# Performance work log

Hardware: AMD Instinct MI355X
Metric: run time of the kernel (lower is better)

## Reference

```python
import jax, jax.numpy as jnp
import numpy as np

HIDDEN = 768
MLP_HIDDEN = 3072
HEADS = 12
HEAD_DIM = HIDDEN // HEADS

def setup_inputs() -> dict:
    key = jax.random.key(0)
    ks = jax.random.split(key, 12)
    s = 0.02
    return {
        "x": jax.random.normal(ks[0], (16, 1024, HIDDEN), dtype=jnp.float32),
        "ln1_g": jnp.ones((HIDDEN,), jnp.float32),
        "ln1_b": jnp.zeros((HIDDEN,), jnp.float32),
        "wq": jax.random.normal(ks[1], (HIDDEN, HIDDEN), jnp.float32) * s,
        "wk": jax.random.normal(ks[2], (HIDDEN, HIDDEN), jnp.float32) * s,
        "wv": jax.random.normal(ks[3], (HIDDEN, HIDDEN), jnp.float32) * s,
        "wo": jax.random.normal(ks[4], (HIDDEN, HIDDEN), jnp.float32) * s,
        "bo": jnp.zeros((HIDDEN,), jnp.float32),
        "ln2_g": jnp.ones((HIDDEN,), jnp.float32),
        "ln2_b": jnp.zeros((HIDDEN,), jnp.float32),
        "w1": jax.random.normal(ks[5], (HIDDEN, MLP_HIDDEN), jnp.float32) * s,
        "b1": jnp.zeros((MLP_HIDDEN,), jnp.float32),
        "w2": jax.random.normal(ks[6], (MLP_HIDDEN, HIDDEN), jnp.float32) * s,
        "b2": jnp.zeros((HIDDEN,), jnp.float32),
    }

def _layernorm(x, g, b, eps=1e-5):
    mu = jnp.mean(x, axis=-1, keepdims=True)
    var = jnp.mean(jnp.square(x - mu), axis=-1, keepdims=True)
    return (x - mu) * jax.lax.rsqrt(var + eps) * g + b

def reference(x, ln1_g, ln1_b, wq, wk, wv, wo, bo, ln2_g, ln2_b, w1, b1, w2, b2):
    b, n, _ = x.shape
    h, d = HEADS, HEAD_DIM
    scale = d ** -0.5
    # Attention branch
    xn = _layernorm(x, ln1_g, ln1_b)
    q = (xn @ wq.T).reshape(b, n, h, d).transpose(0, 2, 1, 3)  # bhnd
    k = (xn @ wk.T).reshape(b, n, h, d).transpose(0, 2, 1, 3)
    v = (xn @ wv.T).reshape(b, n, h, d).transpose(0, 2, 1, 3)
    score = jax.nn.softmax(jnp.einsum('bhif,bhjf->bhij', q, k) * scale, axis=-1)
    attn = jnp.einsum('bhij,bhjf->bihf', score, v).reshape(b, n, h * d)
    x = attn @ wo.T + bo + x
    # MLP branch
    xn = _layernorm(x, ln2_g, ln2_b)
    hdn = jax.nn.gelu(xn @ w1 + b1, approximate=False)
    x = hdn @ w2 + b2 + x
    return x
```

## Files before the change

### kernel.cpp

```cpp
#include <hip/hip_runtime.h>
#include <hip/hip_bf16.h>

#define HIDDEN 768
#define MLPH   3072
#define HEADS  12
#define HD     64
#define SEQ    1024
#define BATCH  16
#define MTOT   (BATCH*SEQ)

typedef __attribute__((ext_vector_type(8))) short  short8;
typedef __attribute__((ext_vector_type(8))) __bf16 bf16x8;
typedef __attribute__((ext_vector_type(4))) float  floatx4;

#define CL2 0.18033688011112042f

__device__ inline short f2bf(float f) {
  __hip_bfloat16 h = __float2bfloat16(f);
  return *reinterpret_cast<short*>(&h);
}

__device__ inline floatx4 mfma_bf16(short8 a, short8 b, floatx4 c) {
  return __builtin_amdgcn_mfma_f32_16x16x32_bf16(
      __builtin_bit_cast(bf16x8, a), __builtin_bit_cast(bf16x8, b), c, 0, 0, 0);
}

__device__ inline void gl_lds16(const short* g, short* l) {
  __builtin_amdgcn_global_load_lds(
      (const __attribute__((address_space(1))) unsigned int*)g,
      (__attribute__((address_space(3))) unsigned int*)l, 16, 0, 0);
}

__global__ __launch_bounds__(256) void conv_weights(
    const float* __restrict__ wq, const float* __restrict__ wk,
    const float* __restrict__ wv, const float* __restrict__ wo,
    const float* __restrict__ w1, const float* __restrict__ w2,
    short* __restrict__ wqkvb, short* __restrict__ wob,
    short* __restrict__ w1t,   short* __restrict__ w2t)
{
  int i = blockIdx.x * 256 + threadIdx.x;
  const int HH = HIDDEN * HIDDEN;
  if (i < HH) {
    wqkvb[i]        = f2bf(wq[i]);
    wqkvb[HH + i]   = f2bf(wk[i]);
    wqkvb[2*HH + i] = f2bf(wv[i]);
    wob[i]          = f2bf(wo[i]);
  }
  if (i < HIDDEN * MLPH) {
    int n = i / HIDDEN, k = i % HIDDEN;
    w1t[i] = f2bf(w1[(size_t)k * MLPH + n]);
    int n2 = i / MLPH, k2 = i % MLPH;
    w2t[i] = f2bf(w2[(size_t)k2 * HIDDEN + n2]);
  }
}

__global__ __launch_bounds__(256) void ln_kernel(
    const float* __restrict__ x, const float* __restrict__ g,
    const float* __restrict__ b, short* __restrict__ out)
{
  int row = blockIdx.x;
  const float* xr = x + (size_t)row * HIDDEN;
  int t = threadIdx.x;
  float v0 = xr[t], v1 = xr[t + 256], v2 = xr[t + 512];
  float s  = v0 + v1 + v2;
  float s2 = v0*v0 + v1*v1 + v2*v2;
  for (int off = 32; off > 0; off >>= 1) {
    s  += __shfl_down(s, off);
    s2 += __shfl_down(s2, off);
  }
  __shared__ float red[8];
  __shared__ float stats[2];
  int wave = t >> 6;
  if ((t & 63) == 0) { red[wave] = s; red[4 + wave] = s2; }
  __syncthreads();
  if (t == 0) {
    float S  = red[0] + red[1] + red[2] + red[3];
    float S2 = red[4] + red[5] + red[6] + red[7];
    float mu  = S * (1.0f / HIDDEN);
    float var = S2 * (1.0f / HIDDEN) - mu * mu;
    stats[0] = mu;
    stats[1] = rsqrtf(var + 1e-5f);
  }
  __syncthreads();
  float mu = stats[0], rs = stats[1];
  short* orow = out + (size_t)row * HIDDEN;
  orow[t]       = f2bf((v0 - mu) * rs * g[t]       + b[t]);
  orow[t + 256] = f2bf((v1 - mu) * rs * g[t + 256] + b[t + 256]);
  orow[t + 512] = f2bf((v2 - mu) * rs * g[t + 512] + b[t + 512]);
}

template<int OUTMODE , bool BIAS, bool GELU_E, bool RES,
         bool SCALEQ = false>
__global__ __launch_bounds__(512, 2) void gemm_bt2(
    const short* __restrict__ A, const short* __restrict__ B,
    const float* __restrict__ bias, const float* __restrict__ res,
    void* __restrict__ out, int M, int N, int K)
{
  __shared__ alignas(16) short As[2][8192];
  __shared__ alignas(16) short Bs[2][8192];

  int tid = threadIdx.x;
  int lane = tid & 63, wave = tid >> 6;
  int wr = wave >> 2, wc = wave & 3;
  int quad = lane >> 4, lc = lane & 15;

  int nbx = gridDim.x;
  int nwg = nbx * gridDim.y;
  int orig = blockIdx.y * nbx + blockIdx.x;
  int q8 = nwg >> 3, r8 = nwg & 7;
  int xcd = orig & 7, sub = orig >> 3;
  int wg = (xcd < r8 ? xcd * (q8 + 1) : r8 * (q8 + 1) + (xcd - r8) * q8) + sub;
  int m0 = (wg / nbx) * 256;
  int n0 = (wg % nbx) * 256;

  int srow = tid >> 2;
  int skb  = (tid & 3) ^ ((srow >> 1) & 3);
  const short* ga0 = A + (size_t)(m0 + srow) * K + skb * 8;
  const short* ga1 = ga0 + (size_t)128 * K;
  const short* gb0 = B + (size_t)(n0 + srow) * K + skb * 8;
  const short* gb1 = gb0 + (size_t)128 * K;
  int lbase = wave * 512;

#define STAGE(KO, BUF) {                              \
    gl_lds16(ga0 + (KO), &As[BUF][lbase]);            \
    gl_lds16(ga1 + (KO), &As[BUF][4096 + lbase]);     \
    gl_lds16(gb0 + (KO), &Bs[BUF][lbase]);            \
    gl_lds16(gb1 + (KO), &Bs[BUF][4096 + lbase]);     \
  }

  floatx4 acc[8][4];
#pragma unroll
  for (int i = 0; i < 8; ++i)
#pragma unroll
    for (int j = 0; j < 4; ++j) acc[i][j] = floatx4{0.f, 0.f, 0.f, 0.f};

  int apos = (quad ^ ((lc >> 1) & 3)) * 8;
  int arow = wr * 128 + lc;
  int brow = wc * 64 + lc;

#define COMPUTE(BUF) {                                                  \
    const short* as_ = As[BUF];                                         \
    const short* bs_ = Bs[BUF];                                         \
    short8 af[8], bfr[4];                                               \
    _Pragma("unroll")                                                   \
    for (int i = 0; i < 8; ++i)                                         \
      af[i] = *(const short8*)&as_[(arow + i * 16) * 32 + apos];        \
    _Pragma("unroll")                                                   \
    for (int j = 0; j < 4; ++j)                                         \
      bfr[j] = *(const short8*)&bs_[(brow + j * 16) * 32 + apos];       \
    _Pragma("unroll")                                                   \
    for (int i = 0; i < 8; ++i)                                         \
      _Pragma("unroll")                                                 \
      for (int j = 0; j < 4; ++j)                                       \
        acc[i][j] = mfma_bf16(af[i], bfr[j], acc[i][j]);                \
  }

  int NT = K >> 5;

  STAGE(0, 0);
  __syncthreads();

  for (int t = 0; t < NT; t += 2) {
    STAGE((t + 1) * 32, 1);
    COMPUTE(0);
    __syncthreads();
    if (t + 2 < NT) STAGE((t + 2) * 32, 0);
    COMPUTE(1);
    __syncthreads();
  }
#undef STAGE
#undef COMPUTE

#pragma unroll
  for (int i = 0; i < 8; ++i)
#pragma unroll
    for (int j = 0; j < 4; ++j)
#pragma unroll
      for (int r = 0; r < 4; ++r) {
        int row = m0 + wr * 128 + i * 16 + quad * 4 + r;
        int col = n0 + wc * 64 + j * 16 + lc;
        float v = acc[i][j][r];
        if (BIAS)   v += bias[col];
        if (GELU_E) v = 0.5f * v * (1.0f + erff(v * 0.70710678118f));
        if (RES)    v += res[(size_t)row * N + col];
        if (SCALEQ && col < HIDDEN) v *= CL2;
        if (OUTMODE == 1) ((short*)out)[(size_t)row * N + col] = f2bf(v);
        else              ((float*)out)[(size_t)row * N + col] = v;
      }
}

__global__ __launch_bounds__(256) void attn_kernel(
    const short* __restrict__ qkv, short* __restrict__ out)
{
  int qt = blockIdx.x;
  int h  = blockIdx.y;
  int b  = blockIdx.z;
  int tid = threadIdx.x, lane = tid & 63, wave = tid >> 6;
  int quad = lane >> 4, lc = lane & 15;

  __shared__ alignas(16) short Qs[2 * 64 * 32];
  __shared__ alignas(16) short Ks[2 * 64 * 32];
  __shared__ alignas(16) unsigned int Vt[64 * 32];
  __shared__ alignas(16) short Ps[4][16 * 64];

  const int LDQ = 3 * HIDDEN;
  const short* qb = qkv + (size_t)(b * SEQ) * LDQ + h * HD;
  const short* kb = qb + HIDDEN;
  const short* vb = qb + 2 * HIDDEN;

  {
    int r_l = lane >> 2, lcb = lane & 3;
    int kblk = lcb ^ ((r_l >> 1) & 3);
#pragma unroll
    for (int t = 0; t < 2; ++t) {
      const short* g = qb + (size_t)(qt * 64 + wave * 16 + r_l) * LDQ + t * 32 + kblk * 8;
      gl_lds16(g, &Qs[t * 2048 + (wave * 16) * 32]);
    }
  }
  __syncthreads();

  short8 aq[2];
#pragma unroll
  for (int ks = 0; ks < 2; ++ks) {
    int pos = quad ^ ((lc >> 1) & 3);
    aq[ks] = *(const short8*)&Qs[ks * 2048 + (wave * 16 + lc) * 32 + pos * 8];
  }

  floatx4 oacc[4];
#pragma unroll
  for (int n2 = 0; n2 < 4; ++n2) oacc[n2] = floatx4{0.f, 0.f, 0.f, 0.f};
  float l_r[4] = {0.f, 0.f, 0.f, 0.f};

  int rt = tid >> 3;
  int ct = tid & 7;

  for (int kt = 0; kt < 16; ++kt) {
    {
      int r_l = lane >> 2, lcb = lane & 3;
      int kblk = lcb ^ ((r_l >> 1) & 3);
#pragma unroll
      for (int t = 0; t < 2; ++t) {
        const short* g = kb + (size_t)(kt * 64 + wave * 16 + r_l) * LDQ + t * 32 + kblk * 8;
        gl_lds16(g, &Ks[t * 2048 + (wave * 16) * 32]);
      }
      const short* gv = vb + (size_t)(kt * 64 + 2 * rt) * LDQ + ct * 8;
      short8 v0 = *(const short8*)(gv);
      short8 v1 = *(const short8*)(gv + LDQ);
      int posv = (rt >> 2) ^ ct;
#pragma unroll
      for (int j = 0; j < 8; ++j) {
        unsigned int d = ((unsigned int)(unsigned short)v1[j] << 16) |
                          (unsigned int)(unsigned short)v0[j];
        Vt[(ct * 8 + j) * 32 + posv * 4 + (rt & 3)] = d;
      }
    }
    __syncthreads();

    floatx4 sacc[4];
#pragma unroll
    for (int n2 = 0; n2 < 4; ++n2) sacc[n2] = floatx4{0.f, 0.f, 0.f, 0.f};
#pragma unroll
    for (int ks = 0; ks < 2; ++ks) {
#pragma unroll
      for (int n2 = 0; n2 < 4; ++n2) {
        int pos = quad ^ ((lc >> 1) & 3);
        short8 bk = *(const short8*)&Ks[ks * 2048 + (n2 * 16 + lc) * 32 + pos * 8];
        sacc[n2] = mfma_bf16(aq[ks], bk, sacc[n2]);
      }
    }

#pragma unroll
    for (int r = 0; r < 4; ++r) {
      int row = quad * 4 + r;
      float p0 = exp2f(sacc[0][r]);
      float p1 = exp2f(sacc[1][r]);
      float p2 = exp2f(sacc[2][r]);
      float p3 = exp2f(sacc[3][r]);
      l_r[r] += (p0 + p1) + (p2 + p3);
      float pv[4] = {p0, p1, p2, p3};
#pragma unroll
      for (int n2 = 0; n2 < 4; ++n2) {
        int tbw  = 2 * n2 + (lc >> 3);
        int posw = tbw ^ (row & 7);
        Ps[wave][row * 64 + posw * 8 + (lc & 7)] = f2bf(pv[n2]);
      }
    }
    __syncthreads();

#pragma unroll
    for (int ks = 0; ks < 2; ++ks) {
      int posp = (ks * 4 + quad) ^ (lc & 7);
      short8 ap = *(const short8*)&Ps[wave][lc * 64 + posp * 8];
#pragma unroll
      for (int n2 = 0; n2 < 4; ++n2) {
        int c = n2 * 16 + lc;
        int posr = ((ks * 4 + quad) ^ ((c >> 3) & 7));
        short8 bv = *(const short8*)&Vt[c * 32 + posr * 4];
        oacc[n2] = mfma_bf16(ap, bv, oacc[n2]);
      }
    }
    __syncthreads();
  }

#pragma unroll
  for (int r = 0; r < 4; ++r) {
    float rs = l_r[r];
#pragma unroll
    for (int off = 1; off < 16; off <<= 1)
      rs += __shfl_xor(rs, off);
    float inv = 1.0f / rs;
    int row = b * SEQ + qt * 64 + wave * 16 + quad * 4 + r;
#pragma unroll
    for (int n2 = 0; n2 < 4; ++n2) {
      int col = h * HD + n2 * 16 + lc;
      out[(size_t)row * HIDDEN + col] = f2bf(oacc[n2][r] * inv);
    }
  }
}

extern "C" void kernel_launch(void* const* d_in, const int* in_sizes, int n_in,
                              void* d_out, int out_size, void* d_ws, size_t ws_size,
                              hipStream_t stream) {
  const float* x    = (const float*)d_in[0];
  const float* ln1g = (const float*)d_in[1];
  const float* ln1b = (const float*)d_in[2];
  const float* wq   = (const float*)d_in[3];
  const float* wk   = (const float*)d_in[4];
  const float* wv   = (const float*)d_in[5];
  const float* wo   = (const float*)d_in[6];
  const float* bo   = (const float*)d_in[7];
  const float* ln2g = (const float*)d_in[8];
  const float* ln2b = (const float*)d_in[9];
  const float* w1   = (const float*)d_in[10];
  const float* b1   = (const float*)d_in[11];
  const float* w2   = (const float*)d_in[12];
  const float* b2   = (const float*)d_in[13];

  auto rup = [](size_t b) { return (b + 255) & ~(size_t)255; };
  const size_t wbytes = rup((size_t)3 * HIDDEN * HIDDEN * 2) +
                        rup((size_t)HIDDEN * HIDDEN * 2) +
                        rup((size_t)MLPH * HIDDEN * 2) +
                        rup((size_t)HIDDEN * MLPH * 2);

  int R = SEQ;
  const int cands[4] = {16384, 8192, 4096, 2048};
  for (int i = 0; i < 4; ++i) {
    size_t need = wbytes + rup((size_t)cands[i] * 1536) + rup((size_t)cands[i] * 6144);
    if (need <= ws_size) { R = cands[i]; break; }
  }

  char* ws = (char*)d_ws;
  size_t off = 0;
  auto alloc = [&](size_t bytes) {
    char* p = ws + off;
    off += (bytes + 255) & ~(size_t)255;
    return p;
  };
  short* wqkvb = (short*)alloc((size_t)3 * HIDDEN * HIDDEN * 2);
  short* wob   = (short*)alloc((size_t)HIDDEN * HIDDEN * 2);
  short* w1t   = (short*)alloc((size_t)MLPH * HIDDEN * 2);
  short* w2t   = (short*)alloc((size_t)HIDDEN * MLPH * 2);
  short* slotA = (short*)alloc((size_t)R * 1536);
  short* bigR  = (short*)alloc((size_t)R * 6144);

  conv_weights<<<(HIDDEN * MLPH + 255) / 256, 256, 0, stream>>>(
      wq, wk, wv, wo, w1, w2, wqkvb, wob, w1t, w2t);

  const int nch = MTOT / R;
  for (int c = 0; c < nch; ++c) {
    const float* xc  = x + (size_t)c * R * HIDDEN;
    float*       x2c = (float*)d_out + (size_t)c * R * HIDDEN;

    ln_kernel<<<R, 256, 0, stream>>>(xc, ln1g, ln1b, slotA);
    gemm_bt2<1, false, false, false, true>
        <<<dim3((3 * HIDDEN) / 256, R / 256), 512, 0, stream>>>(
        slotA, wqkvb, nullptr, nullptr, bigR, R, 3 * HIDDEN, HIDDEN);
    attn_kernel<<<dim3(SEQ / 64, HEADS, R / SEQ), 256, 0, stream>>>(bigR, slotA);
    gemm_bt2<0, true, false, true>
        <<<dim3(HIDDEN / 256, R / 256), 512, 0, stream>>>(
        slotA, wob, bo, xc, x2c, R, HIDDEN, HIDDEN);
    ln_kernel<<<R, 256, 0, stream>>>(x2c, ln2g, ln2b, slotA);
    gemm_bt2<1, true, true, false>
        <<<dim3(MLPH / 256, R / 256), 512, 0, stream>>>(
        slotA, w1t, b1, nullptr, bigR, R, MLPH, HIDDEN);
    gemm_bt2<0, true, false, true>
        <<<dim3(HIDDEN / 256, R / 256), 512, 0, stream>>>(
        bigR, w2t, b2, x2c, x2c, R, HIDDEN, MLPH);
  }
}
```

Measured before the change: 628.4 us.

## Pre-transpose V in a separate kernel and widen attention blocks to 128 queries

Adds a vtrans kernel that writes V per (batch, head, key tile) into a swizzled, transposed layout in workspace. The attention kernel can then load it with direct global-to-LDS copies instead of doing scalar in-kernel transposes. The attention block grows to 512 threads covering 128 query rows, so each K/V tile is shared by twice as many waves. The S tile is computed transposed, so each lane's P values go to its own wave-private LDS buffer with a single vector store and no block barrier. This costs an extra kernel launch, extra workspace and an extra read and write of V through global memory.

Measured after the change: 616.9 us. Within noise of the previous version (-1.8%).

```diff
diff --git a/kernel.cpp b/kernel.cpp
--- a/kernel.cpp
+++ b/kernel.cpp
@@ -10,6 +10,7 @@
 #define MTOT   (BATCH*SEQ)
 
 typedef __attribute__((ext_vector_type(8))) short  short8;
+typedef __attribute__((ext_vector_type(4))) short  short4x;
 typedef __attribute__((ext_vector_type(8))) __bf16 bf16x8;
 typedef __attribute__((ext_vector_type(4))) float  floatx4;
 
@@ -189,8 +190,42 @@
       }
 }
 
-__global__ __launch_bounds__(256) void attn_kernel(
-    const short* __restrict__ qkv, short* __restrict__ out)
+__global__ __launch_bounds__(256) void vtrans_kernel(
+    const short* __restrict__ qkv, short* __restrict__ vtg)
+{
+  int kt = blockIdx.x, h = blockIdx.y, b = blockIdx.z;
+  int t = threadIdx.x;
+  __shared__ short Vl[64][72];
+  const short* vb = qkv + (size_t)(b * SEQ + kt * 64) * 2304 + 1536 + h * 64;
+  int row = t >> 2, seg = t & 3;
+  short8 r0 = *(const short8*)(vb + (size_t)row * 2304 + seg * 16);
+  short8 r1 = *(const short8*)(vb + (size_t)row * 2304 + seg * 16 + 8);
+  *(short8*)&Vl[row][seg * 16]     = r0;
+  *(short8*)&Vl[row][seg * 16 + 8] = r1;
+  __syncthreads();
+  int ks = t >> 7, d = (t & 127) >> 1, hb = t & 1;
+  short8 w0;
+#pragma unroll
+  for (int u = 0; u < 8; ++u) {
+    int blk = hb * 2 + (u >> 3), j = u & 7;
+    int ksrc = ks * 32 + (blk ^ ((d >> 1) & 3)) * 8 + j;
+    w0[u] = Vl[ksrc][d];
+  }
+  short8 w1;
+#pragma unroll
+  for (int u = 8; u < 16; ++u) {
+    int blk = hb * 2 + (u >> 3), j = u & 7;
+    int ksrc = ks * 32 + (blk ^ ((d >> 1) & 3)) * 8 + j;
+    w1[u - 8] = Vl[ksrc][d];
+  }
+  short* o = vtg + ((size_t)((b * HEADS + h) * 16 + kt)) * 4096 + t * 16;
+  *(short8*)o       = w0;
+  *(short8*)(o + 8) = w1;
+}
+
+__global__ __launch_bounds__(512) void attn_kernel(
+    const short* __restrict__ qkv, const short* __restrict__ vtg,
+    short* __restrict__ out)
 {
   int qt = blockIdx.x;
   int h  = blockIdx.y;
@@ -198,118 +233,95 @@
   int tid = threadIdx.x, lane = tid & 63, wave = tid >> 6;
   int quad = lane >> 4, lc = lane & 15;
 
-  __shared__ alignas(16) short Qs[2 * 64 * 32];
+  __shared__ alignas(16) short Qs[2 * 128 * 32];
   __shared__ alignas(16) short Ks[2 * 64 * 32];
-  __shared__ alignas(16) unsigned int Vt[64 * 32];
-  __shared__ alignas(16) short Ps[4][16 * 64];
+  __shared__ alignas(16) short Vs[2 * 64 * 32];
+  __shared__ alignas(16) short Ps[8][16 * 72];
 
   const int LDQ = 3 * HIDDEN;
   const short* qb = qkv + (size_t)(b * SEQ) * LDQ + h * HD;
   const short* kb = qb + HIDDEN;
-  const short* vb = qb + 2 * HIDDEN;
+  const short* vt = vtg + (size_t)((b * HEADS + h) * 16) * 4096;
 
   {
-    int r_l = lane >> 2, lcb = lane & 3;
-    int kblk = lcb ^ ((r_l >> 1) & 3);
+    int row = tid >> 2, blk = tid & 3;
+    int kblk = blk ^ ((row >> 1) & 3);
 #pragma unroll
     for (int t = 0; t < 2; ++t) {
-      const short* g = qb + (size_t)(qt * 64 + wave * 16 + r_l) * LDQ + t * 32 + kblk * 8;
-      gl_lds16(g, &Qs[t * 2048 + (wave * 16) * 32]);
+      const short* g = qb + (size_t)(qt * 128 + row) * LDQ + t * 32 + kblk * 8;
+      gl_lds16(g, &Qs[t * 4096 + wave * 512]);
     }
   }
   __syncthreads();
 
+  int pos = quad ^ ((lc >> 1) & 3);
   short8 aq[2];
 #pragma unroll
-  for (int ks = 0; ks < 2; ++ks) {
-    int pos = quad ^ ((lc >> 1) & 3);
-    aq[ks] = *(const short8*)&Qs[ks * 2048 + (wave * 16 + lc) * 32 + pos * 8];
-  }
+  for (int ks = 0; ks < 2; ++ks)
+    aq[ks] = *(const short8*)&Qs[ks * 4096 + (wave * 16 + lc) * 32 + pos * 8];
 
   floatx4 oacc[4];
 #pragma unroll
   for (int n2 = 0; n2 < 4; ++n2) oacc[n2] = floatx4{0.f, 0.f, 0.f, 0.f};
-  float l_r[4] = {0.f, 0.f, 0.f, 0.f};
-
-  int rt = tid >> 3;
-  int ct = tid & 7;
+  float lsum = 0.f;
+
+  int srow = (tid >> 2) & 63;
+  int sks  = tid >> 8;
+  int skb  = (tid & 3) ^ ((srow >> 1) & 3);
+  const short* kg0 = kb + (size_t)srow * LDQ + sks * 32 + skb * 8;
+  const short* vg0 = vt + tid * 8;
+  short* pw = &Ps[wave][0];
 
   for (int kt = 0; kt < 16; ++kt) {
-    {
-      int r_l = lane >> 2, lcb = lane & 3;
-      int kblk = lcb ^ ((r_l >> 1) & 3);
-#pragma unroll
-      for (int t = 0; t < 2; ++t) {
-        const short* g = kb + (size_t)(kt * 64 + wave * 16 + r_l) * LDQ + t * 32 + kblk * 8;
-        gl_lds16(g, &Ks[t * 2048 + (wave * 16) * 32]);
-      }
-      const short* gv = vb + (size_t)(kt * 64 + 2 * rt) * LDQ + ct * 8;
-      short8 v0 = *(const short8*)(gv);
-      short8 v1 = *(const short8*)(gv + LDQ);
-      int posv = (rt >> 2) ^ ct;
-#pragma unroll
-      for (int j = 0; j < 8; ++j) {
-        unsigned int d = ((unsigned int)(unsigned short)v1[j] << 16) |
-                          (unsigned int)(unsigned short)v0[j];
-        Vt[(ct * 8 + j) * 32 + posv * 4 + (rt & 3)] = d;
+    gl_lds16(kg0 + (size_t)(kt * 64) * LDQ, &Ks[wave * 512]);
+    gl_lds16(vg0 + kt * 4096, &Vs[wave * 512]);
+    __syncthreads();
+
+    floatx4 sacc[4];
+#pragma unroll
+    for (int m2 = 0; m2 < 4; ++m2) sacc[m2] = floatx4{0.f, 0.f, 0.f, 0.f};
+#pragma unroll
+    for (int ks = 0; ks < 2; ++ks) {
+#pragma unroll
+      for (int m2 = 0; m2 < 4; ++m2) {
+        short8 ak = *(const short8*)&Ks[ks * 2048 + (m2 * 16 + lc) * 32 + pos * 8];
+        sacc[m2] = mfma_bf16(ak, aq[ks], sacc[m2]);
       }
     }
-    __syncthreads();
-
-    floatx4 sacc[4];
-#pragma unroll
-    for (int n2 = 0; n2 < 4; ++n2) sacc[n2] = floatx4{0.f, 0.f, 0.f, 0.f};
+
+#pragma unroll
+    for (int m2 = 0; m2 < 4; ++m2) {
+      float p0 = exp2f(sacc[m2][0]);
+      float p1 = exp2f(sacc[m2][1]);
+      float p2 = exp2f(sacc[m2][2]);
+      float p3 = exp2f(sacc[m2][3]);
+      lsum += (p0 + p1) + (p2 + p3);
+      short4x pk;
+      pk[0] = f2bf(p0); pk[1] = f2bf(p1); pk[2] = f2bf(p2); pk[3] = f2bf(p3);
+      *(short4x*)&pw[lc * 72 + m2 * 16 + quad * 4] = pk;
+    }
+    asm volatile("s_waitcnt lgkmcnt(0)" ::: "memory");
+    __builtin_amdgcn_sched_barrier(0);
+
 #pragma unroll
     for (int ks = 0; ks < 2; ++ks) {
+      short8 ap = *(const short8*)&pw[lc * 72 + (ks * 4 + quad) * 8];
 #pragma unroll
       for (int n2 = 0; n2 < 4; ++n2) {
-        int pos = quad ^ ((lc >> 1) & 3);
-        short8 bk = *(const short8*)&Ks[ks * 2048 + (n2 * 16 + lc) * 32 + pos * 8];
-        sacc[n2] = mfma_bf16(aq[ks], bk, sacc[n2]);
-      }
-    }
-
-#pragma unroll
-    for (int r = 0; r < 4; ++r) {
-      int row = quad * 4 + r;
-      float p0 = exp2f(sacc[0][r]);
-      float p1 = exp2f(sacc[1][r]);
-      float p2 = exp2f(sacc[2][r]);
-      float p3 = exp2f(sacc[3][r]);
-      l_r[r] += (p0 + p1) + (p2 + p3);
-      float pv[4] = {p0, p1, p2, p3};
-#pragma unroll
-      for (int n2 = 0; n2 < 4; ++n2) {
-        int tbw  = 2 * n2 + (lc >> 3);
-        int posw = tbw ^ (row & 7);
-        Ps[wave][row * 64 + posw * 8 + (lc & 7)] = f2bf(pv[n2]);
-      }
-    }
-    __syncthreads();
-
-#pragma unroll
-    for (int ks = 0; ks < 2; ++ks) {
-      int posp = (ks * 4 + quad) ^ (lc & 7);
-      short8 ap = *(const short8*)&Ps[wave][lc * 64 + posp * 8];
-#pragma unroll
-      for (int n2 = 0; n2 < 4; ++n2) {
-        int c = n2 * 16 + lc;
-        int posr = ((ks * 4 + quad) ^ ((c >> 3) & 7));
-        short8 bv = *(const short8*)&Vt[c * 32 + posr * 4];
+        short8 bv = *(const short8*)&Vs[ks * 2048 + (n2 * 16 + lc) * 32 + pos * 8];
         oacc[n2] = mfma_bf16(ap, bv, oacc[n2]);
       }
     }
     __syncthreads();
   }
 
+  float rs = lsum;
+  rs += __shfl_xor(rs, 16);
+  rs += __shfl_xor(rs, 32);
 #pragma unroll
   for (int r = 0; r < 4; ++r) {
-    float rs = l_r[r];
-#pragma unroll
-    for (int off = 1; off < 16; off <<= 1)
-      rs += __shfl_xor(rs, off);
-    float inv = 1.0f / rs;
-    int row = b * SEQ + qt * 64 + wave * 16 + quad * 4 + r;
+    float inv = 1.0f / __shfl(rs, quad * 4 + r);
+    int row = b * SEQ + qt * 128 + wave * 16 + quad * 4 + r;
 #pragma unroll
     for (int n2 = 0; n2 < 4; ++n2) {
       int col = h * HD + n2 * 16 + lc;
@@ -345,7 +357,8 @@
   int R = SEQ;
   const int cands[4] = {16384, 8192, 4096, 2048};
   for (int i = 0; i < 4; ++i) {
-    size_t need = wbytes + rup((size_t)cands[i] * 1536) + rup((size_t)cands[i] * 6144);
+    size_t need = wbytes + rup((size_t)cands[i] * 1536) + rup((size_t)cands[i] * 6144)
+                         + rup((size_t)cands[i] * 1536);
     if (need <= ws_size) { R = cands[i]; break; }
   }
 
@@ -362,6 +375,7 @@
   short* w2t   = (short*)alloc((size_t)HIDDEN * MLPH * 2);
   short* slotA = (short*)alloc((size_t)R * 1536);
   short* bigR  = (short*)alloc((size_t)R * 6144);
+  short* vtg   = (short*)alloc((size_t)R * 1536);
 
   conv_weights<<<(HIDDEN * MLPH + 255) / 256, 256, 0, stream>>>(
       wq, wk, wv, wo, w1, w2, wqkvb, wob, w1t, w2t);
@@ -375,7 +389,9 @@
     gemm_bt2<1, false, false, false, true>
         <<<dim3((3 * HIDDEN) / 256, R / 256), 512, 0, stream>>>(
         slotA, wqkvb, nullptr, nullptr, bigR, R, 3 * HIDDEN, HIDDEN);
-    attn_kernel<<<dim3(SEQ / 64, HEADS, R / SEQ), 256, 0, stream>>>(bigR, slotA);
+    vtrans_kernel<<<dim3(16, HEADS, R / SEQ), 256, 0, stream>>>(bigR, vtg);
+    attn_kernel<<<dim3(SEQ / 128, HEADS, R / SEQ), 512, 0, stream>>>(
+        bigR, vtg, slotA);
     gemm_bt2<0, true, false, true>
         <<<dim3(HIDDEN / 256, R / 256), 512, 0, stream>>>(
         slotA, wob, bo, xc, x2c, R, HIDDEN, HIDDEN);
```
